# Kernel tuning notes

Measured on AMD Instinct MI355X. Metric: run time of the kernel, lower is better.

The kernel has to match this reference:

```python
import jax, jax.numpy as jnp
import numpy as np
from jax import lax

BS, L, HID = 16, 512, 768
H, HD, NREG = 12, 64, 8
R2 = 2 * NREG


def setup_inputs() -> dict:
    key = jax.random.key(0)
    ks = jax.random.split(key, 7)
    s = 1.0 / np.sqrt(HID)
    return {
        "hidden_states": jax.random.normal(ks[0], (BS, L, HID), jnp.float32),
        "K1_w": jax.random.normal(ks[1], (H * HD, HID), jnp.float32) * s,
        "K1_b": jnp.zeros((H * HD,), jnp.float32),
        "V1_w": jax.random.normal(ks[2], (H * HD, HID), jnp.float32) * s,
        "V1_b": jnp.zeros((H * HD,), jnp.float32),
        "reading_head": jax.random.normal(ks[3], (H, HD), jnp.float32) * (1.0 / np.sqrt(HD)),
        "bidirection_weight": jnp.ones((1, 1, H, 1, R2), jnp.float32) * (1.0 / R2),
    }


def _softmax_dim1(x):
    # torch: softmax over length dim (1) plus 1/exp(max) residual term
    m = jnp.max(x, axis=1, keepdims=True)
    e = jnp.exp(x - m)
    return e / jnp.sum(e, axis=1, keepdims=True) + jnp.exp(-m)


def _cummax_idx(e):
    # torch.cummax indices over axis=1 for a bool tensor (ties -> latest index):
    # last True index so far; if no True yet, current index.
    ar = jnp.arange(e.shape[1], dtype=jnp.int32)[None, :, None]
    lt = lax.cummax(jnp.where(e, ar, jnp.int32(-1)), axis=1)
    return jnp.where(lt >= 0, lt, ar)


def reference(hidden_states, K1_w, K1_b, V1_w, V1_b, reading_head, bidirection_weight):
    bs, length, _ = hidden_states.shape
    K1 = jax.nn.relu(hidden_states @ K1_w.T + K1_b).reshape(bs, length, H, HD)
    V1 = jax.nn.relu(hidden_states @ V1_w.T + V1_b).reshape(bs, length, H, HD)

    scores = jnp.einsum("blhn,hn->blh", K1, reading_head)
    events = _softmax_dim1(scores) > (1.5 / length)  # (bs, L, H) bool; fwd==bwd for IC1

    col0 = _cummax_idx(events)  # (bs, L, H)
    rolled = jnp.roll(events, -1, axis=1)
    col1 = jnp.flip(512 - _cummax_idx(jnp.flip(rolled, axis=1)), axis=1)
    col1 = col1.at[:, 0].set(0)

    # sequential shift-register scan over length
    e_seq = jnp.moveaxis(events, 1, 0)  # (L, bs, H)
    f_seq = jnp.moveaxis(col0, 1, 0)
    b_seq = jnp.moveaxis(col1, 1, 0)
    row0 = jnp.concatenate(
        [f_seq[0][:, None], b_seq[0][:, None], jnp.zeros((bs, R2, H), jnp.int32)], axis=1
    )  # (bs, R2+2, H)

    def step(row, inp):
        e, f, b = inp
        reg = jnp.where(e[:, None, :], row[:, :-2], row[:, 2:])  # shift-in on event
        new_row = jnp.concatenate([f[:, None], b[:, None], reg], axis=1)
        return new_row, reg

    _, regs = lax.scan(step, row0, (e_seq[1:], f_seq[1:], b_seq[1:]))
    regs = jnp.concatenate([jnp.zeros((1, bs, R2, H), jnp.int32), regs], axis=0)  # (L,bs,R2,H)
    idx = jnp.moveaxis(regs, 0, 1).reshape(bs, length * R2, H)
    idx = jnp.clip(idx, 0, length - 1)

    V2 = jnp.take_along_axis(V1, idx[..., None], axis=1).reshape(bs, length, R2, H, HD)
    w = bidirection_weight.reshape(H, R2)
    return jnp.einsum("blrhd,hr->blhd", V2, w)  # (bs, L, H, HD)
```

## Files before the change

### kernel.cpp

```cpp
#include <hip/hip_runtime.h>
#include <cstdint>
#include <cstddef>

#define BSZ 16
#define LQ  512
#define HIDDIM 768
#define NH  12
#define HD  64
#define R2V 16
#define NTOT 1536
#define MTOT 8192

typedef __bf16 bf16x8 __attribute__((ext_vector_type(8)));
typedef float  f32x4  __attribute__((ext_vector_type(4)));

__device__ inline unsigned short f2bf(float x) {
    union { float f; unsigned u; } c; c.f = x;
    unsigned r = c.u + 0x7fffu + ((c.u >> 16) & 1u);
    return (unsigned short)(r >> 16);
}
__device__ inline float bfl(unsigned u) { return __uint_as_float(u << 16); }
__device__ inline float bfh(unsigned u) { return __uint_as_float(u & 0xffff0000u); }

#define TBM 128
#define TBN 128
#define TBK 32
#define KT  (HIDDIM / TBK)
#define ATILE (TBM * TBK)

#define CVT8(dstp, f0, f1) do {                                               \
        bf16x8 t_;                                                            \
        t_[0] = (__bf16)(f0).x; t_[1] = (__bf16)(f0).y;                       \
        t_[2] = (__bf16)(f0).z; t_[3] = (__bf16)(f0).w;                       \
        t_[4] = (__bf16)(f1).x; t_[5] = (__bf16)(f1).y;                       \
        t_[6] = (__bf16)(f1).z; t_[7] = (__bf16)(f1).w;                       \
        *reinterpret_cast<bf16x8*>(dstp) = t_;                                \
    } while (0)

__global__ __launch_bounds__(256, 3) void gemm_mfma(
    const float* __restrict__ hs,
    const float* __restrict__ Kw,
    const float* __restrict__ Vw,
    const float* __restrict__ Kb, const float* __restrict__ Vb,
    unsigned short* __restrict__ K1b, unsigned short* __restrict__ V1b)
{
    __shared__ unsigned short As[2][ATILE];
    __shared__ unsigned short Bs[2][ATILE];

    const int wg  = blockIdx.y * 12 + blockIdx.x;
    const int nid = (wg & 7) * 96 + (wg >> 3);
    const int bx  = nid % 12;
    const int by  = nid / 12;
    const int n0  = bx * TBN;
    const int m0  = by * TBM;

    const bool isK = (n0 < HIDDIM);
    const float* __restrict__ Wsrc = isK ? Kw : Vw;
    const int nsub = isK ? 0 : HIDDIM;
    const int nb0  = n0 - nsub;

    const int tid  = threadIdx.x;
    const int wid  = tid >> 6;
    const int lane = tid & 63;
    const int wm   = (wid & 1) * 64;
    const int wn   = (wid >> 1) * 64;

    f32x4 acc[4][4] = {};

    const int rr = lane >> 1;
    const int kh = lane & 1;
    const int r0 = wid * 32;
    const int ra = r0 + rr;
    const int sw = (ra >> 1) & 3;
    const int u0 = ((2 * kh) ^ sw) * 8;
    const int u1 = ((2 * kh + 1) ^ sw) * 8;

    const float* Ag = hs   + (size_t)(m0  + ra) * HIDDIM + kh * 16;
    const float* Bg = Wsrc + (size_t)(nb0 + ra) * HIDDIM + kh * 16;

    const int fm   = lane & 15;
    const int fj   = lane >> 4;
    const int koff = ((fj ^ ((fm >> 1) & 3)) << 3);

    float4 a0, a1, a2, a3, b0, b1, b2, b3;

#define LOADG(kt) do {                                                        \
        const float4* pa_ = (const float4*)(Ag + (kt) * TBK);                 \
        a0 = pa_[0]; a1 = pa_[1]; a2 = pa_[2]; a3 = pa_[3];                   \
        const float4* pb_ = (const float4*)(Bg + (kt) * TBK);                 \
        b0 = pb_[0]; b1 = pb_[1]; b2 = pb_[2]; b3 = pb_[3];                   \
    } while (0)

#define CVTWRITE(buf) do {                                                    \
        CVT8(&As[buf][ra * TBK + u0], a0, a1);                                \
        CVT8(&As[buf][ra * TBK + u1], a2, a3);                                \
        CVT8(&Bs[buf][ra * TBK + u0], b0, b1);                                \
        CVT8(&Bs[buf][ra * TBK + u1], b2, b3);                                \
    } while (0)

    LOADG(0);
    CVTWRITE(0);
    LOADG(1);
    asm volatile("s_waitcnt lgkmcnt(0)" ::: "memory");
    __builtin_amdgcn_sched_barrier(0);

    for (int kt = 0; kt < KT; ++kt) {
        __builtin_amdgcn_s_barrier();
        __builtin_amdgcn_sched_barrier(0);
        const int cb = kt & 1;

        if (kt + 1 < KT) {
            CVTWRITE(cb ^ 1);
            if (kt + 2 < KT) LOADG(kt + 2);
        }

        bf16x8 af[4], bfr[4];
        #pragma unroll
        for (int mi = 0; mi < 4; ++mi)
            af[mi] = *reinterpret_cast<const bf16x8*>(
                &As[cb][(wm + mi * 16 + fm) * TBK + koff]);
        #pragma unroll
        for (int ni = 0; ni < 4; ++ni)
            bfr[ni] = *reinterpret_cast<const bf16x8*>(
                &Bs[cb][(wn + ni * 16 + fm) * TBK + koff]);
        __builtin_amdgcn_s_setprio(1);
        #pragma unroll
        for (int mi = 0; mi < 4; ++mi)
            #pragma unroll
            for (int ni = 0; ni < 4; ++ni)
                acc[mi][ni] = __builtin_amdgcn_mfma_f32_16x16x32_bf16(
                    bfr[ni], af[mi], acc[mi][ni], 0, 0, 0);
        __builtin_amdgcn_s_setprio(0);
    }
#undef LOADG
#undef CVTWRITE

    unsigned short* __restrict__ dst = isK ? K1b : V1b;
    const float* __restrict__ bsrc   = isK ? Kb : Vb;
    const int nq = fj * 4;

    #pragma unroll
    for (int mi = 0; mi < 4; ++mi) {
        const int mg = m0 + wm + mi * 16 + fm;
        #pragma unroll
        for (int ni = 0; ni < 4; ++ni) {
            const int ng = n0 + wn + ni * 16 + nq;
            float4 bv = *(const float4*)(bsrc + (ng - nsub));
            f32x4 a = acc[mi][ni];
            ushort4 o;
            o.x = f2bf(fmaxf(a[0] + bv.x, 0.f));
            o.y = f2bf(fmaxf(a[1] + bv.y, 0.f));
            o.z = f2bf(fmaxf(a[2] + bv.z, 0.f));
            o.w = f2bf(fmaxf(a[3] + bv.w, 0.f));
            *(ushort4*)(dst + (size_t)mg * HIDDIM + (ng - nsub)) = o;
        }
    }
}

#define SINF (1 << 30)
#define IXP 17

__global__ __launch_bounds__(512) void scan_gather(
    const unsigned short* __restrict__ K1b,
    const unsigned short* __restrict__ V1b,
    const float* __restrict__ rh,
    const float* __restrict__ bw,
    float* __restrict__ out)
{
    const int bh   = blockIdx.x >> 2;
    const int part = blockIdx.x & 3;
    const int b    = bh / NH;
    const int h    = bh % NH;
    const int l    = threadIdx.x;
    const int lane = l & 63;
    const int wid  = l >> 6;

    __shared__ float wredA[8];
    __shared__ float wredB[8];
    __shared__ int   wp0[8];
    __shared__ int   wp1[8];
    __shared__ int   wp2[8];
    __shared__ int   ev[LQ];
    __shared__ int   col0[LQ];
    __shared__ int   col1[LQ];
    __shared__ int   E[LQ];
    __shared__ int   idxs[LQ * IXP];
    __shared__ float wsm[R2V];

    if (l < R2V) wsm[l] = bw[h * R2V + l];

    const unsigned short* krow = K1b + ((size_t)(b * LQ + l)) * HIDDIM + h * HD;
    const float* rrow = rh + h * HD;
    float s = 0.f;
    #pragma unroll
    for (int c8 = 0; c8 < 8; ++c8) {
        uint4 kv = *(const uint4*)(krow + c8 * 8);
        float4 ra = *(const float4*)(rrow + c8 * 8);
        float4 rb = *(const float4*)(rrow + c8 * 8 + 4);
        s += bfl(kv.x) * ra.x + bfh(kv.x) * ra.y
           + bfl(kv.y) * ra.z + bfh(kv.y) * ra.w
           + bfl(kv.z) * rb.x + bfh(kv.z) * rb.y
           + bfl(kv.w) * rb.z + bfh(kv.w) * rb.w;
    }

    float mx = s;
    #pragma unroll
    for (int off = 32; off > 0; off >>= 1) mx = fmaxf(mx, __shfl_xor(mx, off));
    if (lane == 0) wredA[wid] = mx;
    __syncthreads();
    float m = wredA[0];
    #pragma unroll
    for (int i = 1; i < 8; ++i) m = fmaxf(m, wredA[i]);

    const float e = expf(s - m);
    float sm = e;
    #pragma unroll
    for (int off = 32; off > 0; off >>= 1) sm += __shfl_xor(sm, off);
    if (lane == 0) wredB[wid] = sm;
    __syncthreads();
    float ssum = 0.f;
    #pragma unroll
    for (int i = 0; i < 8; ++i) ssum += wredB[i];

    const float p = e / ssum + expf(-m);
    const int event = (p > (1.5f / 512.0f)) ? 1 : 0;
    ev[l] = event;

    int v = event ? l : -1;
    #pragma unroll
    for (int off = 1; off < 64; off <<= 1) {
        int u = __shfl_up(v, off);
        if (lane >= off) v = (u > v) ? u : v;
    }
    if (lane == 63) wp0[wid] = v;
    __syncthreads();
    int pfx = -1;
    for (int i = 0; i < wid; ++i) pfx = (wp0[i] > pfx) ? wp0[i] : pfx;
    v = (pfx > v) ? pfx : v;
    col0[l] = (v >= 0) ? v : l;

    int v1 = ev[(l + 1) & (LQ - 1)] ? l : SINF;
    #pragma unroll
    for (int off = 1; off < 64; off <<= 1) {
        int u = __shfl_down(v1, off);
        if (lane < 64 - off) v1 = (u < v1) ? u : v1;
    }
    if (lane == 0) wp1[wid] = v1;
    __syncthreads();
    int sfx = SINF;
    for (int i = wid + 1; i < 8; ++i) sfx = (wp1[i] < sfx) ? wp1[i] : sfx;
    v1 = (sfx < v1) ? sfx : v1;
    col1[l] = (l == 0) ? 0 : (((v1 < SINF) ? v1 : l) + 1);

    int c = (l >= 1) ? event : 0;
    #pragma unroll
    for (int off = 1; off < 64; off <<= 1) {
        int u = __shfl_up(c, off);
        if (lane >= off) c += u;
    }
    if (lane == 63) wp2[wid] = c;
    __syncthreads();
    for (int i = 0; i < wid; ++i) c += wp2[i];

    if (l >= 1 && event) E[c - 1] = l;
    __syncthreads();

    int* op = &idxs[l * IXP];
    #pragma unroll
    for (int j = 0; j < 8; ++j) {
        const int k = c - 1 - j;
        int f = 0, bb = 0;
        if (k >= 0) {
            const int t = E[k];
            f  = col0[t - 1];
            bb = col1[t - 1];
        }
        op[2 * j]     = min(max(f, 0), LQ - 1);
        op[2 * j + 1] = min(max(bb, 0), LQ - 1);
    }
    __syncthreads();

    const int dsl = lane & 7;
    const size_t vbase = (size_t)b * LQ * HIDDIM + h * HD + dsl * 8;

    for (int rr = 0; rr < 2; ++rr) {
        const int round = part * 2 + rr;
        const int lg = round * 64 + wid * 8 + (lane >> 3);
        const int* ip = &idxs[lg * IXP];
        float a0 = 0.f, a1 = 0.f, a2 = 0.f, a3 = 0.f;
        float a4 = 0.f, a5 = 0.f, a6 = 0.f, a7 = 0.f;
        #pragma unroll 1
        for (int rc = 0; rc < R2V; rc += 4) {
            const int i0 = ip[rc], i1 = ip[rc + 1], i2 = ip[rc + 2], i3 = ip[rc + 3];
            uint4 v0 = *(const uint4*)(V1b + vbase + (size_t)i0 * HIDDIM);
            uint4 vA = *(const uint4*)(V1b + vbase + (size_t)i1 * HIDDIM);
            uint4 vB = *(const uint4*)(V1b + vbase + (size_t)i2 * HIDDIM);
            uint4 vC = *(const uint4*)(V1b + vbase + (size_t)i3 * HIDDIM);
            const float w0 = wsm[rc], w1 = wsm[rc + 1], w2 = wsm[rc + 2], w3 = wsm[rc + 3];
            a0 += w0 * bfl(v0.x); a1 += w0 * bfh(v0.x);
            a2 += w0 * bfl(v0.y); a3 += w0 * bfh(v0.y);
            a4 += w0 * bfl(v0.z); a5 += w0 * bfh(v0.z);
            a6 += w0 * bfl(v0.w); a7 += w0 * bfh(v0.w);
            a0 += w1 * bfl(vA.x); a1 += w1 * bfh(vA.x);
            a2 += w1 * bfl(vA.y); a3 += w1 * bfh(vA.y);
            a4 += w1 * bfl(vA.z); a5 += w1 * bfh(vA.z);
            a6 += w1 * bfl(vA.w); a7 += w1 * bfh(vA.w);
            a0 += w2 * bfl(vB.x); a1 += w2 * bfh(vB.x);
            a2 += w2 * bfl(vB.y); a3 += w2 * bfh(vB.y);
            a4 += w2 * bfl(vB.z); a5 += w2 * bfh(vB.z);
            a6 += w2 * bfl(vB.w); a7 += w2 * bfh(vB.w);
            a0 += w3 * bfl(vC.x); a1 += w3 * bfh(vC.x);
            a2 += w3 * bfl(vC.y); a3 += w3 * bfh(vC.y);
            a4 += w3 * bfl(vC.z); a5 += w3 * bfh(vC.z);
            a6 += w3 * bfl(vC.w); a7 += w3 * bfh(vC.w);
        }
        float* po = out + ((size_t)(b * LQ + lg) * NH + h) * HD + dsl * 8;
        *(float4*)po       = make_float4(a0, a1, a2, a3);
        *((float4*)po + 1) = make_float4(a4, a5, a6, a7);
    }
}

extern "C" void kernel_launch(void* const* d_in, const int* in_sizes, int n_in,
                              void* d_out, int out_size, void* d_ws, size_t ws_size,
                              hipStream_t stream)
{
    (void)in_sizes; (void)n_in; (void)out_size; (void)ws_size;

    const float* hs = (const float*)d_in[0];
    const float* Kw = (const float*)d_in[1];
    const float* Kb = (const float*)d_in[2];
    const float* Vw = (const float*)d_in[3];
    const float* Vb = (const float*)d_in[4];
    const float* rh = (const float*)d_in[5];
    const float* bw = (const float*)d_in[6];
    float* out = (float*)d_out;

    char* ws = (char*)d_ws;
    unsigned short* K1b = (unsigned short*)(ws);
    unsigned short* V1b = (unsigned short*)(ws + 12582912);

    dim3 g1(NTOT / TBN, MTOT / TBM);
    gemm_mfma<<<g1, 256, 0, stream>>>(hs, Kw, Vw, Kb, Vb, K1b, V1b);

    scan_gather<<<BSZ * NH * 4, LQ, 0, stream>>>(K1b, V1b, rh, bw, out);
}
```

Measured before the change: 150.7 us.

## Stage fp32 tiles via direct global-to-LDS loads, convert to bf16 at fragment read

The GEMM's operand staging now uses global_load_lds DMA to copy fp32 tiles directly into shared memory with an XOR swizzle, instead of loading into registers, converting to bf16 and writing to LDS. Conversion to bf16 moves to the fragment-read step. This removes VGPR staging and the explicit LDS stores. In exchange, LDS use doubles because tiles are stored as fp32, occupancy drops from 3 to 2 blocks, LDS read traffic and conversion work per MFMA rise, and an extra barrier is added per k-step.

```diff
diff --git a/kernel.cpp b/kernel.cpp
--- a/kernel.cpp
+++ b/kernel.cpp
@@ -28,24 +28,19 @@
 #define KT  (HIDDIM / TBK)
 #define ATILE (TBM * TBK)
 
-#define CVT8(dstp, f0, f1) do {                                               \
-        bf16x8 t_;                                                            \
-        t_[0] = (__bf16)(f0).x; t_[1] = (__bf16)(f0).y;                       \
-        t_[2] = (__bf16)(f0).z; t_[3] = (__bf16)(f0).w;                       \
-        t_[4] = (__bf16)(f1).x; t_[5] = (__bf16)(f1).y;                       \
-        t_[6] = (__bf16)(f1).z; t_[7] = (__bf16)(f1).w;                       \
-        *reinterpret_cast<bf16x8*>(dstp) = t_;                                \
-    } while (0)
-
-__global__ __launch_bounds__(256, 3) void gemm_mfma(
+#define GLD16(g, l) __builtin_amdgcn_global_load_lds( \
+    (const __attribute__((address_space(1))) void*)(g), \
+    (__attribute__((address_space(3))) void*)(l), 16, 0, 0)
+
+__global__ __launch_bounds__(256, 2) void gemm_mfma(
     const float* __restrict__ hs,
     const float* __restrict__ Kw,
     const float* __restrict__ Vw,
     const float* __restrict__ Kb, const float* __restrict__ Vb,
     unsigned short* __restrict__ K1b, unsigned short* __restrict__ V1b)
 {
-    __shared__ unsigned short As[2][ATILE];
-    __shared__ unsigned short Bs[2][ATILE];
+    __shared__ float As[2][ATILE];
+    __shared__ float Bs[2][ATILE];
 
     const int wg  = blockIdx.y * 12 + blockIdx.x;
     const int nid = (wg & 7) * 96 + (wg >> 3);
@@ -67,62 +62,62 @@
 
     f32x4 acc[4][4] = {};
 
-    const int rr = lane >> 1;
-    const int kh = lane & 1;
-    const int r0 = wid * 32;
-    const int ra = r0 + rr;
-    const int sw = (ra >> 1) & 3;
-    const int u0 = ((2 * kh) ^ sw) * 8;
-    const int u1 = ((2 * kh + 1) ^ sw) * 8;
-
-    const float* Ag = hs   + (size_t)(m0  + ra) * HIDDIM + kh * 16;
-    const float* Bg = Wsrc + (size_t)(nb0 + ra) * HIDDIM + kh * 16;
-
-    const int fm   = lane & 15;
-    const int fj   = lane >> 4;
-    const int koff = ((fj ^ ((fm >> 1) & 3)) << 3);
-
-    float4 a0, a1, a2, a3, b0, b1, b2, b3;
-
-#define LOADG(kt) do {                                                        \
-        const float4* pa_ = (const float4*)(Ag + (kt) * TBK);                 \
-        a0 = pa_[0]; a1 = pa_[1]; a2 = pa_[2]; a3 = pa_[3];                   \
-        const float4* pb_ = (const float4*)(Bg + (kt) * TBK);                 \
-        b0 = pb_[0]; b1 = pb_[1]; b2 = pb_[2]; b3 = pb_[3];                   \
+    const int r0   = wid * 32;
+    const int sr   = lane >> 3;
+    const int scol = ((lane & 7) ^ sr) * 4;
+
+    const float* Agp = hs   + (size_t)(m0  + r0 + sr) * HIDDIM + scol;
+    const float* Bgp = Wsrc + (size_t)(nb0 + r0 + sr) * HIDDIM + scol;
+
+#define STAGE(buf, kt) do {                                                   \
+        const int kof_ = (kt) * TBK;                                          \
+        _Pragma("unroll")                                                     \
+        for (int j_ = 0; j_ < 4; ++j_) {                                      \
+            GLD16(Agp + (size_t)(8 * j_) * HIDDIM + kof_,                     \
+                  &As[buf][(r0 + 8 * j_) * TBK]);                             \
+            GLD16(Bgp + (size_t)(8 * j_) * HIDDIM + kof_,                     \
+                  &Bs[buf][(r0 + 8 * j_) * TBK]);                             \
+        }                                                                     \
     } while (0)
 
-#define CVTWRITE(buf) do {                                                    \
-        CVT8(&As[buf][ra * TBK + u0], a0, a1);                                \
-        CVT8(&As[buf][ra * TBK + u1], a2, a3);                                \
-        CVT8(&Bs[buf][ra * TBK + u0], b0, b1);                                \
-        CVT8(&Bs[buf][ra * TBK + u1], b2, b3);                                \
+    const int fm = lane & 15;
+    const int fj = lane >> 4;
+    const int s8 = fm & 7;
+    const int u0 = ((2 * fj)     ^ s8) * 4;
+    const int u1 = ((2 * fj + 1) ^ s8) * 4;
+
+#define RDFRAG(dstv, base, row) do {                                          \
+        const float4 p_ = *(const float4*)(&(base)[(row) * TBK + u0]);        \
+        const float4 q_ = *(const float4*)(&(base)[(row) * TBK + u1]);        \
+        (dstv)[0] = (__bf16)p_.x; (dstv)[1] = (__bf16)p_.y;                   \
+        (dstv)[2] = (__bf16)p_.z; (dstv)[3] = (__bf16)p_.w;                   \
+        (dstv)[4] = (__bf16)q_.x; (dstv)[5] = (__bf16)q_.y;                   \
+        (dstv)[6] = (__bf16)q_.z; (dstv)[7] = (__bf16)q_.w;                   \
     } while (0)
 
-    LOADG(0);
-    CVTWRITE(0);
-    LOADG(1);
-    asm volatile("s_waitcnt lgkmcnt(0)" ::: "memory");
+    STAGE(0, 0);
+    asm volatile("s_waitcnt vmcnt(0)" ::: "memory");
+    __builtin_amdgcn_s_barrier();
     __builtin_amdgcn_sched_barrier(0);
 
     for (int kt = 0; kt < KT; ++kt) {
+        if (kt + 1 < KT) {
+            STAGE((kt + 1) & 1, kt + 1);
+            asm volatile("s_waitcnt vmcnt(8)" ::: "memory");
+        } else {
+            asm volatile("s_waitcnt vmcnt(0)" ::: "memory");
+        }
         __builtin_amdgcn_s_barrier();
         __builtin_amdgcn_sched_barrier(0);
         const int cb = kt & 1;
 
-        if (kt + 1 < KT) {
-            CVTWRITE(cb ^ 1);
-            if (kt + 2 < KT) LOADG(kt + 2);
-        }
-
         bf16x8 af[4], bfr[4];
         #pragma unroll
         for (int mi = 0; mi < 4; ++mi)
-            af[mi] = *reinterpret_cast<const bf16x8*>(
-                &As[cb][(wm + mi * 16 + fm) * TBK + koff]);
+            RDFRAG(af[mi], As[cb], wm + mi * 16 + fm);
         #pragma unroll
         for (int ni = 0; ni < 4; ++ni)
-            bfr[ni] = *reinterpret_cast<const bf16x8*>(
-                &Bs[cb][(wn + ni * 16 + fm) * TBK + koff]);
+            RDFRAG(bfr[ni], Bs[cb], wn + ni * 16 + fm);
         __builtin_amdgcn_s_setprio(1);
         #pragma unroll
         for (int mi = 0; mi < 4; ++mi)
@@ -131,9 +126,11 @@
                 acc[mi][ni] = __builtin_amdgcn_mfma_f32_16x16x32_bf16(
                     bfr[ni], af[mi], acc[mi][ni], 0, 0, 0);
         __builtin_amdgcn_s_setprio(0);
-    }
-#undef LOADG
-#undef CVTWRITE
+        __builtin_amdgcn_sched_barrier(0);
+        __builtin_amdgcn_s_barrier();
+    }
+#undef STAGE
+#undef RDFRAG
 
     unsigned short* __restrict__ dst = isK ? K1b : V1b;
     const float* __restrict__ bsrc   = isK ? Kb : Vb;
```

Result: slower. 164.5 us (+9.1%).
